# Kernel tuning notes

Hardware: AMD Instinct MI355X
Metric: run time of the kernel (lower is better)

## Reference

```python
import jax, jax.numpy as jnp
import numpy as np

NUM_JOINTS = 140
NUM_VERTICES = 13059
NUM_BONES = 28
BATCH = 512


def euler_zyx_to_rot(e):
    """e: [..., 3] Euler angles in (z, y, x) order -> [..., 3, 3] with R = Rz @ Ry @ Rx."""
    z, y, x = e[..., 0], e[..., 1], e[..., 2]
    cx, sx = jnp.cos(x), jnp.sin(x)
    cy, sy = jnp.cos(y), jnp.sin(y)
    cz, sz = jnp.cos(z), jnp.sin(z)
    r00 = cz * cy
    r01 = cz * sy * sx - sz * cx
    r02 = cz * sy * cx + sz * sx
    r10 = sz * cy
    r11 = sz * sy * sx + cz * cx
    r12 = sz * sy * cx - cz * sx
    r20 = -sy
    r21 = cy * sx
    r22 = cy * cx
    R = jnp.stack([r00, r01, r02, r10, r11, r12, r20, r21, r22], axis=-1)
    return R.reshape(e.shape[:-1] + (3, 3))


def _mouse_forward(pose, bone_lengths, center_bone_length, trans, scale,
                   v_template, t_pose_joints, weights, parent, bone_mapper):
    B = pose.shape[0]
    Jn = NUM_JOINTS
    dt = pose.dtype

    bl = jax.nn.sigmoid(bone_lengths / 5.0) * 2.0            # [B, 28]
    R = euler_zyx_to_rot(pose.reshape(B, Jn, 3))             # [B, J, 3, 3]
    Jt = t_pose_joints                                       # [J, 3]

    # bone offsets for joints 1..J-1, scaled per bone_length_mapper
    off = Jt[1:] - Jt[parent[1:]]                            # [J-1, 3]
    blid = bone_mapper[1:]                                   # [J-1]
    bl_g = jnp.where(blid[None, :] >= 0,
                     jnp.take(bl, jnp.maximum(blid, 0), axis=1),
                     jnp.ones((), dt))                       # [B, J-1]
    # joint index 1 (position 0 in the [J-1] arrays) uses center_bone_length
    scale_per = bl_g.at[:, 0].set(center_bone_length[:, 0])
    off_b = off[None] * scale_per[..., None]                 # [B, J-1, 3]

    bottom = jnp.broadcast_to(jnp.array([0., 0., 0., 1.], dt), (B, Jn - 1, 1, 4))
    top = jnp.concatenate([R[:, 1:], off_b[..., None]], axis=-1)   # [B, J-1, 3, 4]
    A = jnp.concatenate([top, bottom], axis=-2)              # [B, J-1, 4, 4] local transforms

    root_t = jnp.broadcast_to(Jt[0], (B, 3))[..., None]      # [B, 3, 1]
    root_top = jnp.concatenate([R[:, 0], root_t], axis=-1)   # [B, 3, 4]
    root_bot = jnp.broadcast_to(jnp.array([0., 0., 0., 1.], dt), (B, 1, 4))
    G0 = jnp.concatenate([root_top, root_bot], axis=-2)      # [B, 4, 4]

    G_init = jnp.zeros((B, Jn, 4, 4), dt).at[:, 0].set(G0)

    def step(G, xs):
        i, p, Ai = xs                                        # Ai: [B, 4, 4]
        Gp = jnp.take(G, p, axis=1)                          # [B, 4, 4]
        Gi = Gp @ Ai
        return G.at[:, i].set(Gi), None

    idx = jnp.arange(1, Jn)
    G, _ = jax.lax.scan(step, G_init, (idx, parent[1:], jnp.swapaxes(A, 0, 1)))

    J_final = G[:, :, :3, 3]                                 # [B, J, 3]

    # subtract rest-pose joint contribution (relative transforms for LBS)
    Jh = jnp.concatenate([jnp.broadcast_to(Jt, (B, Jn, 3)),
                          jnp.zeros((B, Jn, 1), dt)], axis=-1)      # [B, J, 4]
    d = jnp.einsum('bjmn,bjn->bjm', G, Jh)                   # [B, J, 4]
    G_rel = jnp.concatenate([G[..., :3], (G[..., 3] - d)[..., None]], axis=-1)

    # linear blend skinning
    T = jnp.einsum('vj,bjmn->bvmn', weights, G_rel)          # [B, V, 4, 4]
    vh = jnp.concatenate([v_template, jnp.ones((NUM_VERTICES, 1), dt)], axis=-1)
    V = jnp.einsum('bvmn,vn->bvm', T[:, :, :3, :], vh)       # [B, V, 3]

    s = scale[:, 0][:, None, None]
    V = V * s + trans[:, None, :]
    J_out = J_final * s + trans[:, None, :]
    return V, J_out


def setup_inputs() -> dict:
    key = jax.random.key(0)
    ks = jax.random.split(key, 8)
    rng = np.random.default_rng(0)
    parent = np.zeros(NUM_JOINTS, dtype=np.int32)
    for i in range(1, NUM_JOINTS):
        parent[i] = rng.integers(0, i)                       # valid kinematic tree
    bone_mapper = rng.integers(-1, NUM_BONES, size=NUM_JOINTS).astype(np.int32)
    W = jax.random.uniform(ks[6], (NUM_VERTICES, NUM_JOINTS), jnp.float32)
    W = W / jnp.sum(W, axis=1, keepdims=True)                # row-stochastic skinning weights
    return {
        'pose': jax.random.normal(ks[0], (BATCH, NUM_JOINTS * 3), jnp.float32) * 0.2,
        'bone_lengths': jax.random.normal(ks[1], (BATCH, NUM_BONES), jnp.float32),
        'center_bone_length': jax.random.uniform(ks[2], (BATCH, 1), jnp.float32, 0.5, 1.5),
        'trans': jax.random.normal(ks[3], (BATCH, 3), jnp.float32),
        'scale': jax.random.uniform(ks[4], (BATCH, 1), jnp.float32, 0.5, 1.5),
        'v_template': jax.random.normal(ks[5], (NUM_VERTICES, 3), jnp.float32),
        't_pose_joints': jax.random.normal(ks[7], (NUM_JOINTS, 3), jnp.float32),
        'weights': W,
        'parent': jnp.asarray(parent),
        'bone_mapper': jnp.asarray(bone_mapper),
    }


def reference(pose, bone_lengths, center_bone_length, trans, scale,
              v_template, t_pose_joints, weights, parent, bone_mapper):
    return _mouse_forward(pose, bone_lengths, center_bone_length, trans, scale,
                          v_template, t_pose_joints, weights, parent, bone_mapper)
```

## Files before the change

kernel.cpp:

```cpp
#include <hip/hip_runtime.h>
#include <math.h>

#define NJ 140
#define NV 13059
#define NB 512
#define NBONES 28

#define MTILES 103
#define NBLK 12
#define KS 18
#define GRID_GEMM (MTILES*NBLK)

#define APREP_SLOTS (MTILES*KS*512)

typedef _Float16 f16x8 __attribute__((ext_vector_type(8)));
typedef float    f32x4 __attribute__((ext_vector_type(4)));

#define GL16(gp, lp) __builtin_amdgcn_global_load_lds( \
    (const __attribute__((address_space(1))) unsigned int*)(gp), \
    (__attribute__((address_space(3))) unsigned int*)(lp), 16, 0, 0)

__global__ __launch_bounds__(256) void prep_kernel(
    const float* __restrict__ pose,
    const float* __restrict__ bone_lengths,
    const float* __restrict__ cbl,
    const float* __restrict__ trans,
    const float* __restrict__ scale,
    const float* __restrict__ v_template,
    const float* __restrict__ t_pose,
    const int*   __restrict__ parent,
    const int*   __restrict__ bone_mapper,
    const float* __restrict__ weights,
    _Float16* __restrict__ Ap,
    _Float16* __restrict__ Bp,
    float* __restrict__ jout)
{
    const int t = threadIdx.x;

    if (blockIdx.x >= NB) {
        const int id  = blockIdx.x - NB;
        const int mt  = id / KS;
        const int ks  = id - mt*KS;
        const int row = t >> 1;
        const int q   = t & 1;
        const int v   = mt*128 + row;
        const int j0  = ks*8 + q*4;
        const int s   = (row >> 1) & 3;

        f16x8 oA, oB;
        #pragma unroll
        for (int i = 0; i < 8; ++i) { oA[i] = (_Float16)0.f; oB[i] = (_Float16)0.f; }

        if (v < NV && j0 + 3 < NJ) {
            float x = v_template[v*3+0];
            float y = v_template[v*3+1];
            float z = v_template[v*3+2];
            const float4 w4 = *(const float4*)(weights + (size_t)v*NJ + j0);
            oA[0] = (_Float16)(w4.x*x); oA[1] = (_Float16)(w4.x*y);
            oA[2] = (_Float16)(w4.x*z); oA[3] = (_Float16)w4.x;
            oA[4] = (_Float16)(w4.y*x); oA[5] = (_Float16)(w4.y*y);
            oA[6] = (_Float16)(w4.y*z); oA[7] = (_Float16)w4.y;
            oB[0] = (_Float16)(w4.z*x); oB[1] = (_Float16)(w4.z*y);
            oB[2] = (_Float16)(w4.z*z); oB[3] = (_Float16)w4.z;
            oB[4] = (_Float16)(w4.w*x); oB[5] = (_Float16)(w4.w*y);
            oB[6] = (_Float16)(w4.w*z); oB[7] = (_Float16)w4.w;
        }
        const int base = ((2*q) ^ s) & ~1;
        _Float16* dst = Ap + (((size_t)id)*512 + row*4 + base)*8;
        if (s & 1) {
            *(f16x8*)dst       = oB;
            *(f16x8*)(dst + 8) = oA;
        } else {
            *(f16x8*)dst       = oA;
            *(f16x8*)(dst + 8) = oB;
        }
        return;
    }

    __shared__ float M0[NJ][12];
    __shared__ float M1[NJ][12];
    __shared__ int   a0[NJ];
    __shared__ int   a1[NJ];

    const int b = blockIdx.x;

    if (t < NJ) {
        const int j = t;
        float z = pose[b*(NJ*3) + 3*j + 0];
        float y = pose[b*(NJ*3) + 3*j + 1];
        float x = pose[b*(NJ*3) + 3*j + 2];
        float cx = cosf(x), sx = sinf(x);
        float cy = cosf(y), sy = sinf(y);
        float cz = cosf(z), sz = sinf(z);
        float r00 = cz*cy;
        float r01 = cz*sy*sx - sz*cx;
        float r02 = cz*sy*cx + sz*sx;
        float r10 = sz*cy;
        float r11 = sz*sy*sx + cz*cx;
        float r12 = sz*sy*cx - cz*sx;
        float r20 = -sy;
        float r21 = cy*sx;
        float r22 = cy*cx;
        float t0, t1, t2;
        int p = parent[j];
        if (j == 0) {
            t0 = t_pose[0]; t1 = t_pose[1]; t2 = t_pose[2];
        } else {
            float ox = t_pose[3*j+0] - t_pose[3*p+0];
            float oy = t_pose[3*j+1] - t_pose[3*p+1];
            float oz = t_pose[3*j+2] - t_pose[3*p+2];
            float s;
            if (j == 1) {
                s = cbl[b];
            } else {
                int blid = bone_mapper[j];
                if (blid >= 0) {
                    float bv = bone_lengths[b*NBONES + blid];
                    s = 2.0f / (1.0f + expf(-bv*0.2f));
                } else {
                    s = 1.0f;
                }
            }
            t0 = ox*s; t1 = oy*s; t2 = oz*s;
        }
        M0[j][0]=r00; M0[j][1]=r01; M0[j][2]=r02;  M0[j][3]=t0;
        M0[j][4]=r10; M0[j][5]=r11; M0[j][6]=r12;  M0[j][7]=t1;
        M0[j][8]=r20; M0[j][9]=r21; M0[j][10]=r22; M0[j][11]=t2;
        a0[j] = (j == 0) ? -1 : p;
    }
    __syncthreads();

    float* src = &M0[0][0]; float* dst = &M1[0][0];
    int* as = a0; int* ad = a1;
    for (int r = 0; r < 8; ++r) {
        if (t < NJ) {
            int a = as[t];
            const float* Mi = src + t*12;
            float* Do = dst + t*12;
            if (a >= 0) {
                const float* Mp = src + a*12;
                #pragma unroll
                for (int m = 0; m < 3; ++m) {
                    float p0 = Mp[m*4+0], p1 = Mp[m*4+1], p2 = Mp[m*4+2], p3 = Mp[m*4+3];
                    Do[m*4+0] = p0*Mi[0] + p1*Mi[4] + p2*Mi[8];
                    Do[m*4+1] = p0*Mi[1] + p1*Mi[5] + p2*Mi[9];
                    Do[m*4+2] = p0*Mi[2] + p1*Mi[6] + p2*Mi[10];
                    Do[m*4+3] = p0*Mi[3] + p1*Mi[7] + p2*Mi[11] + p3;
                }
                ad[t] = as[a];
            } else {
                #pragma unroll
                for (int e = 0; e < 12; ++e) Do[e] = Mi[e];
                ad[t] = -1;
            }
        }
        __syncthreads();
        float* tf = src; src = dst; dst = tf;
        int* ti = as; as = ad; ad = ti;
    }

    float* grl = dst;
    if (t < NJ) {
        const int j = t;
        const float* G = src + j*12;
        float sb = scale[b];
        float tr0 = trans[b*3+0], tr1 = trans[b*3+1], tr2 = trans[b*3+2];
        float* jo = jout + ((size_t)b*NJ + j)*3;
        jo[0] = G[3]*sb  + tr0;
        jo[1] = G[7]*sb  + tr1;
        jo[2] = G[11]*sb + tr2;
        float jx = t_pose[3*j+0], jy = t_pose[3*j+1], jz = t_pose[3*j+2];
        #pragma unroll
        for (int c = 0; c < 3; ++c) {
            float g0 = G[c*4+0], g1 = G[c*4+1], g2 = G[c*4+2];
            float g3 = G[c*4+3] - (g0*jx + g1*jy + g2*jz);
            grl[j*12 + c*4 + 0] = g0;
            grl[j*12 + c*4 + 1] = g1;
            grl[j*12 + c*4 + 2] = g2;
            grl[j*12 + c*4 + 3] = g3;
        }
    }
    __syncthreads();

    if (t < 216) {
        int c  = t / 72;
        int rr = t - c*72;
        int ks = rr >> 2;
        int ci = rr & 3;
        int nrow = b*3 + c;
        int nbp = nrow >> 7;
        int rl = nrow & 127;
        int j0 = ks*8 + ci*2;
        f16x8 o;
        #pragma unroll
        for (int i = 0; i < 8; ++i) o[i] = (_Float16)0.f;
        if (j0 < NJ) {
            o[0] = (_Float16)grl[j0*12 + c*4 + 0];
            o[1] = (_Float16)grl[j0*12 + c*4 + 1];
            o[2] = (_Float16)grl[j0*12 + c*4 + 2];
            o[3] = (_Float16)grl[j0*12 + c*4 + 3];
        }
        if (j0 + 1 < NJ) {
            o[4] = (_Float16)grl[(j0+1)*12 + c*4 + 0];
            o[5] = (_Float16)grl[(j0+1)*12 + c*4 + 1];
            o[6] = (_Float16)grl[(j0+1)*12 + c*4 + 2];
            o[7] = (_Float16)grl[(j0+1)*12 + c*4 + 3];
        }
        int cs = ci ^ ((rl >> 1) & 3);
        *(f16x8*)(Bp + ((size_t)(nbp*KS + ks)*512 + rl*4 + cs)*8) = o;
    }
}

__global__ __launch_bounds__(256, 4) void gemm_kernel(
    const _Float16* __restrict__ Ap,
    const _Float16* __restrict__ Bp,
    const float* __restrict__ scale,
    const float* __restrict__ trans,
    float* __restrict__ vout)
{
    __shared__ __align__(16) char smem[40960];
    _Float16 (*sA)[4096] = (_Float16(*)[4096])smem;
    _Float16 (*sB)[4096] = (_Float16(*)[4096])(smem + 24576);

    const int t    = threadIdx.x;
    const int lane = t & 63;
    const int wid  = t >> 6;
    const int ln   = lane & 15;
    const int kq   = lane >> 4;
    const int wm   = wid & 1;
    const int wn   = wid >> 1;

    const int q8 = GRID_GEMM >> 3;
    const int r8 = GRID_GEMM & 7;
    const int xcd = blockIdx.x & 7;
    const int idx = blockIdx.x >> 3;
    const int wgid = (xcd < r8 ? xcd*(q8+1) : r8*(q8+1) + (xcd-r8)*q8) + idx;

    const int mt = wgid / NBLK;
    const int nb = wgid - mt*NBLK;

    const _Float16* Ag = Ap + (size_t)mt*(KS*4096);
    const _Float16* Bg = Bp + (size_t)nb*(KS*4096);

    const int c1 = wid*64 + lane;
    const int c2 = c1 + 256;
    const int lb1 = wid*512;
    const int lb2 = 2048 + wid*512;

    const int csl = kq ^ ((ln >> 1) & 3);
    const int rA  = wm*64 + ln;
    const int rB  = wn*64 + ln;
    const int afo = rA*32 + csl*8;
    const int bfo = rB*32 + csl*8;

    f32x4 acc[4][4];
    #pragma unroll
    for (int mi = 0; mi < 4; ++mi)
        #pragma unroll
        for (int ni = 0; ni < 4; ++ni)
            acc[mi][ni] = (f32x4){0.f, 0.f, 0.f, 0.f};

    #define STAGE_A(buf, ksv) do { \
        const _Float16* a_ = Ag + (ksv)*4096; \
        GL16(a_ + c1*8, &sA[buf][lb1]); \
        GL16(a_ + c2*8, &sA[buf][lb2]); } while (0)
    #define STAGE_B(buf, ksv) do { \
        const _Float16* b_ = Bg + (ksv)*4096; \
        GL16(b_ + c1*8, &sB[buf][lb1]); \
        GL16(b_ + c2*8, &sB[buf][lb2]); } while (0)

    auto compute = [&](int ba, int bb) {
        f16x8 af[4], bf[4];
        #pragma unroll
        for (int mi = 0; mi < 4; ++mi)
            af[mi] = *(const f16x8*)&sA[ba][afo + mi*512];
        #pragma unroll
        for (int ni = 0; ni < 4; ++ni)
            bf[ni] = *(const f16x8*)&sB[bb][bfo + ni*512];
        __builtin_amdgcn_s_setprio(1);
        #pragma unroll
        for (int mi = 0; mi < 4; ++mi)
            #pragma unroll
            for (int ni = 0; ni < 4; ++ni)
                acc[mi][ni] = __builtin_amdgcn_mfma_f32_16x16x32_f16(
                    af[mi], bf[ni], acc[mi][ni], 0, 0, 0);
        __builtin_amdgcn_s_setprio(0);
    };

    #define STEP(j, bBn, bAn, bAc, bBc) do { \
        asm volatile("s_waitcnt vmcnt(2)" ::: "memory"); \
        __builtin_amdgcn_s_barrier(); \
        STAGE_B(bBn, (j) + 1); \
        STAGE_A(bAn, (j) + 2); \
        compute(bAc, bBc); } while (0)

    STAGE_B(0, 0);
    STAGE_A(0, 0);
    STAGE_A(1, 1);

    #pragma unroll 1
    for (int i = 0; i < 12; i += 6) {
        STEP(i + 0, 1, 2, 0, 0);
        STEP(i + 1, 0, 0, 1, 1);
        STEP(i + 2, 1, 1, 2, 0);
        STEP(i + 3, 0, 2, 0, 1);
        STEP(i + 4, 1, 0, 1, 0);
        STEP(i + 5, 0, 1, 2, 1);
    }
    STEP(12, 1, 2, 0, 0);
    STEP(13, 0, 0, 1, 1);
    STEP(14, 1, 1, 2, 0);
    STEP(15, 0, 2, 0, 1);
    asm volatile("s_waitcnt vmcnt(2)" ::: "memory");
    __builtin_amdgcn_s_barrier();
    STAGE_B(1, 17);
    compute(1, 0);
    asm volatile("s_waitcnt vmcnt(0)" ::: "memory");
    __builtin_amdgcn_s_barrier();
    compute(2, 1);

    #undef STEP
    #undef STAGE_A
    #undef STAGE_B

    float* Ct    = (float*)smem;
    float* es_l  = (float*)(smem + 33792);
    float* etr_l = (float*)(smem + 34304);

    const int vgA = t/3,        crA = t - 3*vgA;
    const int eB  = t + 256;
    const int vgB = eB/3,       crB = eB - 3*vgB;

    #pragma unroll 1
    for (int h = 0; h < 2; ++h) {
        __syncthreads();
        if (wn == h) {
            #pragma unroll
            for (int mi = 0; mi < 4; ++mi)
                #pragma unroll
                for (int ni = 0; ni < 4; ++ni)
                    *(f32x4*)&Ct[(ni*16 + ln)*132 + wm*64 + mi*16 + kq*4] =
                        acc[mi][ni];
        }
        if (h == 0 && t < 128) {
            int n = nb*128 + t;
            es_l[t]  = scale[n/3];
            etr_l[t] = trans[n];
        }
        __syncthreads();

        const int n0   = nb*128 + h*64;
        const int bq0  = n0/3;
        const int off0 = 3*bq0 - n0;
        const int bqN  = (n0 + 63)/3 - bq0 + 1;

        #pragma unroll 1
        for (int bqi = 0; bqi < bqN; ++bqi) {
            const long long base = (long long)(bq0 + bqi)*(NV*3)
                                 + (long long)mt*384;
            {
                int nrel = off0 + 3*bqi + crA;
                if (nrel >= 0 && nrel < 64 && mt*128 + vgA < NV) {
                    int nf = h*64 + nrel;
                    vout[base + t] =
                        Ct[nrel*132 + vgA]*es_l[nf] + etr_l[nf];
                }
            }
            if (t < 128) {
                int nrel = off0 + 3*bqi + crB;
                if (nrel >= 0 && nrel < 64 && mt*128 + vgB < NV) {
                    int nf = h*64 + nrel;
                    vout[base + eB] =
                        Ct[nrel*132 + vgB]*es_l[nf] + etr_l[nf];
                }
            }
        }
    }
}

extern "C" void kernel_launch(void* const* d_in, const int* in_sizes, int n_in,
                              void* d_out, int out_size, void* d_ws, size_t ws_size,
                              hipStream_t stream) {
    const float* pose         = (const float*)d_in[0];
    const float* bone_lengths = (const float*)d_in[1];
    const float* cbl          = (const float*)d_in[2];
    const float* trans        = (const float*)d_in[3];
    const float* scale        = (const float*)d_in[4];
    const float* v_template   = (const float*)d_in[5];
    const float* t_pose       = (const float*)d_in[6];
    const float* weights      = (const float*)d_in[7];
    const int*   parent       = (const int*)d_in[8];
    const int*   bone_mapper  = (const int*)d_in[9];

    float* vout = (float*)d_out;
    float* jout = vout + (size_t)NB*NV*3;

    _Float16* Ap = (_Float16*)d_ws;
    _Float16* Bp = Ap + (size_t)APREP_SLOTS*8;

    prep_kernel<<<NB + MTILES*KS, 256, 0, stream>>>(
        pose, bone_lengths, cbl, trans, scale, v_template, t_pose,
        parent, bone_mapper, weights, Ap, Bp, jout);

    gemm_kernel<<<GRID_GEMM, 256, 0, stream>>>(Ap, Bp, scale, trans, vout);
}
```

Before: 149.4 us.

## Double GEMM block to 512 threads with 8 waves each computing 64x32 sub-tiles

The GEMM workgroup grows from 4 to 8 waves, and each wave now owns a 64x32 output sub-tile instead of 64x64. Staging becomes one global-to-LDS load per thread per operand, and the wait counts are adjusted to match. The epilogue now writes one element per thread across 384 threads. The aim is more waves per CU to hide latency and fewer accumulator registers per wave, at the cost of each wave reusing its LDS fragments less and doing proportionally more LDS reads per MFMA.

```diff
diff --git a/kernel.cpp b/kernel.cpp
--- a/kernel.cpp
+++ b/kernel.cpp
@@ -211,7 +211,7 @@
     }
 }
 
-__global__ __launch_bounds__(256, 4) void gemm_kernel(
+__global__ __launch_bounds__(512, 6) void gemm_kernel(
     const _Float16* __restrict__ Ap,
     const _Float16* __restrict__ Bp,
     const float* __restrict__ scale,
@@ -242,53 +242,40 @@
     const _Float16* Ag = Ap + (size_t)mt*(KS*4096);
     const _Float16* Bg = Bp + (size_t)nb*(KS*4096);
 
-    const int c1 = wid*64 + lane;
-    const int c2 = c1 + 256;
-    const int lb1 = wid*512;
-    const int lb2 = 2048 + wid*512;
-
     const int csl = kq ^ ((ln >> 1) & 3);
-    const int rA  = wm*64 + ln;
-    const int rB  = wn*64 + ln;
-    const int afo = rA*32 + csl*8;
-    const int bfo = rB*32 + csl*8;
-
-    f32x4 acc[4][4];
+    const int afo = (wm*64 + ln)*32 + csl*8;
+    const int bfo = (wn*32 + ln)*32 + csl*8;
+
+    f32x4 acc[4][2];
     #pragma unroll
     for (int mi = 0; mi < 4; ++mi)
         #pragma unroll
-        for (int ni = 0; ni < 4; ++ni)
+        for (int ni = 0; ni < 2; ++ni)
             acc[mi][ni] = (f32x4){0.f, 0.f, 0.f, 0.f};
 
-    #define STAGE_A(buf, ksv) do { \
-        const _Float16* a_ = Ag + (ksv)*4096; \
-        GL16(a_ + c1*8, &sA[buf][lb1]); \
-        GL16(a_ + c2*8, &sA[buf][lb2]); } while (0)
-    #define STAGE_B(buf, ksv) do { \
-        const _Float16* b_ = Bg + (ksv)*4096; \
-        GL16(b_ + c1*8, &sB[buf][lb1]); \
-        GL16(b_ + c2*8, &sB[buf][lb2]); } while (0)
+    #define STAGE_A(buf, ksv) GL16(Ag + (ksv)*4096 + t*8, &sA[buf][wid*512])
+    #define STAGE_B(buf, ksv) GL16(Bg + (ksv)*4096 + t*8, &sB[buf][wid*512])
 
     auto compute = [&](int ba, int bb) {
-        f16x8 af[4], bf[4];
+        f16x8 af[4], bf[2];
         #pragma unroll
         for (int mi = 0; mi < 4; ++mi)
             af[mi] = *(const f16x8*)&sA[ba][afo + mi*512];
         #pragma unroll
-        for (int ni = 0; ni < 4; ++ni)
+        for (int ni = 0; ni < 2; ++ni)
             bf[ni] = *(const f16x8*)&sB[bb][bfo + ni*512];
         __builtin_amdgcn_s_setprio(1);
         #pragma unroll
         for (int mi = 0; mi < 4; ++mi)
             #pragma unroll
-            for (int ni = 0; ni < 4; ++ni)
+            for (int ni = 0; ni < 2; ++ni)
                 acc[mi][ni] = __builtin_amdgcn_mfma_f32_16x16x32_f16(
                     af[mi], bf[ni], acc[mi][ni], 0, 0, 0);
         __builtin_amdgcn_s_setprio(0);
     };
 
     #define STEP(j, bBn, bAn, bAc, bBc) do { \
-        asm volatile("s_waitcnt vmcnt(2)" ::: "memory"); \
+        asm volatile("s_waitcnt vmcnt(1)" ::: "memory"); \
         __builtin_amdgcn_s_barrier(); \
         STAGE_B(bBn, (j) + 1); \
         STAGE_A(bAn, (j) + 2); \
@@ -311,7 +298,7 @@
     STEP(13, 0, 0, 1, 1);
     STEP(14, 1, 1, 2, 0);
     STEP(15, 0, 2, 0, 1);
-    asm volatile("s_waitcnt vmcnt(2)" ::: "memory");
+    asm volatile("s_waitcnt vmcnt(1)" ::: "memory");
     __builtin_amdgcn_s_barrier();
     STAGE_B(1, 17);
     compute(1, 0);
@@ -327,20 +314,18 @@
     float* es_l  = (float*)(smem + 33792);
     float* etr_l = (float*)(smem + 34304);
 
-    const int vgA = t/3,        crA = t - 3*vgA;
-    const int eB  = t + 256;
-    const int vgB = eB/3,       crB = eB - 3*vgB;
+    const int vgA = t/3, crA = t - 3*vgA;
 
     #pragma unroll 1
     for (int h = 0; h < 2; ++h) {
         __syncthreads();
-        if (wn == h) {
+        if ((wn >> 1) == h) {
             #pragma unroll
             for (int mi = 0; mi < 4; ++mi)
                 #pragma unroll
-                for (int ni = 0; ni < 4; ++ni)
-                    *(f32x4*)&Ct[(ni*16 + ln)*132 + wm*64 + mi*16 + kq*4] =
-                        acc[mi][ni];
+                for (int ni = 0; ni < 2; ++ni)
+                    *(f32x4*)&Ct[((wn&1)*32 + ni*16 + ln)*132
+                                 + wm*64 + mi*16 + kq*4] = acc[mi][ni];
         }
         if (h == 0 && t < 128) {
             int n = nb*128 + t;
@@ -358,20 +343,12 @@
         for (int bqi = 0; bqi < bqN; ++bqi) {
             const long long base = (long long)(bq0 + bqi)*(NV*3)
                                  + (long long)mt*384;
-            {
+            if (t < 384) {
                 int nrel = off0 + 3*bqi + crA;
                 if (nrel >= 0 && nrel < 64 && mt*128 + vgA < NV) {
                     int nf = h*64 + nrel;
                     vout[base + t] =
                         Ct[nrel*132 + vgA]*es_l[nf] + etr_l[nf];
-                }
-            }
-            if (t < 128) {
-                int nrel = off0 + 3*bqi + crB;
-                if (nrel >= 0 && nrel < 64 && mt*128 + vgB < NV) {
-                    int nf = h*64 + nrel;
-                    vout[base + eB] =
-                        Ct[nrel*132 + vgB]*es_l[nf] + etr_l[nf];
                 }
             }
         }
@@ -402,5 +379,5 @@
         pose, bone_lengths, cbl, trans, scale, v_template, t_pose,
         parent, bone_mapper, weights, Ap, Bp, jout);
 
-    gemm_kernel<<<GRID_GEMM, 256, 0, stream>>>(Ap, Bp, scale, trans, vout);
+    gemm_kernel<<<GRID_GEMM, 512, 0, stream>>>(Ap, Bp, scale, trans, vout);
 }
```

Measured after the change: 144.7 us. -3.1%, faster.
